# Kernel optimization log

Hardware: AMD Instinct MI355X
Metric: run time of the kernel (lower is better)

The kernel has to match this reference:

```python
import jax, jax.numpy as jnp
import numpy as np

B, T, D, U = 128, 512, 128, 512


def setup_inputs() -> dict:
    key = jax.random.key(0)
    kx, kwx, kwh = jax.random.split(key, 3)
    x = jax.random.normal(kx, (B, T, D), dtype=jnp.float32)
    Wx = jax.random.normal(kwx, (D, U), dtype=jnp.float32) * (1.0 / np.sqrt(D))
    Wh = jax.random.normal(kwh, (U, U), dtype=jnp.float32) * (1.0 / np.sqrt(U))
    b = jnp.zeros((U,), dtype=jnp.float32)
    return {"x": x, "Wx": Wx, "Wh": Wh, "b": b}


def reference(x, Wx, Wh, b):
    # Elman RNN: h_t = tanh(x_t @ Wx + h_{t-1} @ Wh + b)
    # Faithful to MyRNN(return_sequences=True): TensorArray.stack() -> [T, B, U]
    h0 = jnp.zeros((x.shape[0], Wh.shape[0]), dtype=x.dtype)  # fallback zero initial state
    xs = jnp.swapaxes(x, 0, 1)  # [T, B, D] for scan over time

    def step(h, x_t):
        h_new = jnp.tanh(x_t @ Wx + h @ Wh + b)
        return h_new, h_new

    _, seq = jax.lax.scan(step, h0, xs)
    return seq  # [T, B, U]
```

## Files before the change

kernel.cpp:

```cpp
#include <hip/hip_runtime.h>
#include <stddef.h>
#include <stdint.h>


constexpr int B = 128;
constexpr int T = 512;
constexpr int D = 128;
constexpr int U = 512;

typedef _Float16 f16;
typedef _Float16 f16x2 __attribute__((ext_vector_type(2)));
typedef __fp16   fp16x2 __attribute__((ext_vector_type(2)));
typedef unsigned int u32;
typedef u32 u32x16 __attribute__((ext_vector_type(16)));

union U32H2 { u32 u; f16x2 h; fp16x2 p; };

static __device__ __forceinline__ u32 pk(float a, float b) {
    U32H2 c; c.p = __builtin_amdgcn_cvt_pkrtz(a, b); return c.u;
}

#if __has_builtin(__builtin_amdgcn_fdot2)
static __device__ __forceinline__ float fdot2(u32 a, u32 b, float c) {
    U32H2 x, y; x.u = a; y.u = b;
    return __builtin_amdgcn_fdot2(x.h, y.h, c, false);
}
#else
static __device__ __forceinline__ float fdot2(u32 a, u32 b, float c) {
    U32H2 x, y; x.u = a; y.u = b;
    return c + (float)x.h.x * (float)y.h.x + (float)x.h.y * (float)y.h.y;
}
#endif

static __device__ __forceinline__ float fast_tanh(float x) {
    float e = __expf(2.0f * x);
    return 1.0f - 2.0f * __builtin_amdgcn_rcpf(e + 1.0f);
}

__global__ __launch_bounds__(256) void pgemm_kernel(
    const float* __restrict__ x,
    const float* __restrict__ Wx,
    const float* __restrict__ bias,
    float* __restrict__ P)
{
    __shared__ u32 xs[128][66];
    __shared__ u32 ws[64][132];

    const int rb  = blockIdx.x;
    const int cb  = blockIdx.y;
    const int tid = threadIdx.x;
    const int tr  = tid >> 4;
    const int tcc = tid & 15;

    const float4* x4 = (const float4*)x;
#pragma unroll
    for (int l = 0; l < 16; ++l) {
        int idx = tid + l * 256;
        int r   = idx >> 5;
        int q   = idx & 31;
        int m   = rb * 128 + r;
        int b_  = m & 127;
        int t_  = m >> 7;
        float4 v = x4[((size_t)b_ * T + t_) * 32 + q];
        xs[r][2 * q]     = pk(v.x, v.y);
        xs[r][2 * q + 1] = pk(v.z, v.w);
    }
    const float4* W4 = (const float4*)Wx;
#pragma unroll
    for (int l = 0; l < 8; ++l) {
        int idx = tid + l * 256;
        int kp  = idx >> 5;
        int q   = idx & 31;
        float4 a = W4[(size_t)(2 * kp)     * 128 + cb * 32 + q];
        float4 c = W4[(size_t)(2 * kp + 1) * 128 + cb * 32 + q];
        uint4 w;
        w.x = pk(a.x, c.x); w.y = pk(a.y, c.y);
        w.z = pk(a.z, c.z); w.w = pk(a.w, c.w);
        *(uint4*)&ws[kp][4 * q] = w;
    }
    __syncthreads();

    float acc[8][8];
#pragma unroll
    for (int i = 0; i < 8; ++i)
#pragma unroll
        for (int j = 0; j < 8; ++j) acc[i][j] = 0.f;

#pragma unroll 2
    for (int kp = 0; kp < 64; ++kp) {
        u32 xv[8], wv[8];
#pragma unroll
        for (int i = 0; i < 8; ++i) xv[i] = xs[tr + 16 * i][kp];
#pragma unroll
        for (int j = 0; j < 8; ++j) wv[j] = ws[kp][tcc + 16 * j];
#pragma unroll
        for (int i = 0; i < 8; ++i)
#pragma unroll
            for (int j = 0; j < 8; ++j)
                acc[i][j] = fdot2(xv[i], wv[j], acc[i][j]);
    }

#pragma unroll
    for (int j = 0; j < 8; ++j) {
        int c    = cb * 128 + tcc + 16 * j;
        float bv = bias[c];
#pragma unroll
        for (int i = 0; i < 8; ++i) {
            int m = rb * 128 + tr + 16 * i;
            P[(size_t)m * U + c] = acc[i][j] + bv;
        }
    }
}

__global__ __launch_bounds__(512, 2) void rnn_kernel(
    const float* __restrict__ Wh,
    float* __restrict__ out)
{
    __shared__ __align__(16) u32 WhL[32768];
    __shared__ __align__(16) u32 part[16 * 264];
    __shared__ __align__(16) u32 hbuf[320];

    const int tid = threadIdx.x;
    const int tk  = tid >> 5;
    const int tc  = tid & 31;
    const int b   = blockIdx.x;

    u32x16 W0, W1, W2, W3, W4, W5, W6, W7, W8, W9, W10, W11;
#define LOADW(q)                                                          \
    {                                                                     \
        const float* r0 = Wh + (size_t)((tk * 16 + (q)) * 2) * U + tc;    \
        _Pragma("unroll")                                                 \
        for (int j = 0; j < 16; ++j)                                      \
            W##q[j] = pk(r0[32 * j], r0[U + 32 * j]);                     \
    }
    LOADW(0)  LOADW(1)  LOADW(2)  LOADW(3)
    LOADW(4)  LOADW(5)  LOADW(6)  LOADW(7)
    LOADW(8)  LOADW(9)  LOADW(10) LOADW(11)
#undef LOADW

#pragma unroll
    for (int pl2 = 0; pl2 < 4; ++pl2) {
        const float* r0 = Wh + (size_t)((tk * 16 + 12 + pl2) * 2) * U + tc;
#pragma unroll
        for (int jc = 0; jc < 4; ++jc) {
            uint4 w;
            w.x = pk(r0[32 * (4 * jc + 0)], r0[U + 32 * (4 * jc + 0)]);
            w.y = pk(r0[32 * (4 * jc + 1)], r0[U + 32 * (4 * jc + 1)]);
            w.z = pk(r0[32 * (4 * jc + 2)], r0[U + 32 * (4 * jc + 2)]);
            w.w = pk(r0[32 * (4 * jc + 3)], r0[U + 32 * (4 * jc + 3)]);
            *(uint4*)&WhL[((pl2 * 4 + jc) * 512 + tid) * 4] = w;
        }
    }

    if (tid < 320) hbuf[tid] = 0u;
    __syncthreads();

    float* outb = out + (size_t)b * U;
    f16* hb16 = (f16*)hbuf;
    const int p0    = tid >> 1;
    const int hidx  = 2 * (p0 + 4 * (p0 >> 4)) + (tid & 1);

    float pv0 = 0.f, pv1 = 0.f;
    if (tid < 256) { pv0 = outb[tid]; pv1 = outb[tid + 256]; }

    for (int t = 0; t < T; ++t) {
        int tn = (t + 1 < T) ? (t + 1) : t;
        const float* prown = outb + (size_t)tn * (B * U);
        float nv0 = 0.f, nv1 = 0.f;
        if (tid < 256) { nv0 = prown[tid]; nv1 = prown[tid + 256]; }

        float acc[16];
#pragma unroll
        for (int j = 0; j < 16; ++j) acc[j] = 0.f;

        const uint4* h4p = (const uint4*)&hbuf[20 * tk];

#define DOT16(hq, Wq)                                                     \
        {                                                                 \
            u32 hq_ = (hq);                                               \
            _Pragma("unroll")                                             \
            for (int j = 0; j < 16; ++j)                                  \
                acc[j] = fdot2(hq_, Wq[j], acc[j]);                       \
        }
        { uint4 hv = h4p[0];
          DOT16(hv.x, W0) DOT16(hv.y, W1) DOT16(hv.z, W2) DOT16(hv.w, W3) }
        { uint4 hv = h4p[1];
          DOT16(hv.x, W4) DOT16(hv.y, W5) DOT16(hv.z, W6) DOT16(hv.w, W7) }
        { uint4 hv = h4p[2];
          DOT16(hv.x, W8) DOT16(hv.y, W9) DOT16(hv.z, W10) DOT16(hv.w, W11) }
#undef DOT16

        {
            uint4 hv = h4p[3];
#pragma unroll
            for (int pl2 = 0; pl2 < 4; ++pl2) {
                u32 hq = (pl2 == 0) ? hv.x : (pl2 == 1) ? hv.y
                       : (pl2 == 2) ? hv.z : hv.w;
#pragma unroll
                for (int jc = 0; jc < 4; ++jc) {
                    uint4 w = *(const uint4*)&WhL[((pl2 * 4 + jc) * 512 + tid) * 4];
                    acc[4 * jc + 0] = fdot2(hq, w.x, acc[4 * jc + 0]);
                    acc[4 * jc + 1] = fdot2(hq, w.y, acc[4 * jc + 1]);
                    acc[4 * jc + 2] = fdot2(hq, w.z, acc[4 * jc + 2]);
                    acc[4 * jc + 3] = fdot2(hq, w.w, acc[4 * jc + 3]);
                }
            }
        }

#pragma unroll
        for (int j = 0; j < 8; ++j)
            part[tk * 264 + tc + 32 * j] = pk(acc[j], acc[j + 8]);

        __syncthreads();

        if (tid < 256) {
            float s0 = pv0, s1 = pv1;
#pragma unroll
            for (int i = 0; i < 16; ++i) {
                U32H2 w; w.u = part[i * 264 + tid];
                s0 += (float)w.h.x;
                s1 += (float)w.h.y;
            }
            float h0 = fast_tanh(s0);
            float h1 = fast_tanh(s1);
            float* prow = outb + (size_t)t * (B * U);
            prow[tid]        = h0;
            prow[tid + 256]  = h1;
            hb16[hidx]       = (f16)h0;
            hb16[hidx + 320] = (f16)h1;
        }
        pv0 = nv0; pv1 = nv1;

        __syncthreads();
    }
}

extern "C" void kernel_launch(void* const* d_in, const int* in_sizes, int n_in,
                              void* d_out, int out_size, void* d_ws, size_t ws_size,
                              hipStream_t stream)
{
    (void)d_ws; (void)ws_size; (void)in_sizes; (void)n_in; (void)out_size;
    const float* x    = (const float*)d_in[0];
    const float* Wx   = (const float*)d_in[1];
    const float* Wh   = (const float*)d_in[2];
    const float* bias = (const float*)d_in[3];
    float* out = (float*)d_out;

    pgemm_kernel<<<dim3((T * B) / 128, U / 128), 256, 0, stream>>>(x, Wx, bias, out);
    rnn_kernel<<<B, 512, 0, stream>>>(Wh, out);
}
```

Before: 1.034 ms.

## Widen RNN recurrence to 1024 threads with 64-column groups and pipelined LDS weights

The recurrent kernel now runs 1024 threads per block instead of 512. Each thread holds half as many Wh register values (8 columns instead of 16) and the K dimension is split across 16 groups of 64 columns. LDS weight loads are issued ahead and interleaved with register dot products to hide LDS latency. The cross-group reduction becomes a tree sum, and h is packed with a lane shuffle so the padded hbuf indexing goes away. The aim is more waves to hide latency per serial time step, at the cost of more threads taking part in each barrier.

```diff
diff --git a/kernel.cpp b/kernel.cpp
--- a/kernel.cpp
+++ b/kernel.cpp
@@ -12,7 +12,7 @@
 typedef _Float16 f16x2 __attribute__((ext_vector_type(2)));
 typedef __fp16   fp16x2 __attribute__((ext_vector_type(2)));
 typedef unsigned int u32;
-typedef u32 u32x16 __attribute__((ext_vector_type(16)));
+typedef u32 u32x8 __attribute__((ext_vector_type(8)));
 
 union U32H2 { u32 u; f16x2 h; fp16x2 p; };
 
@@ -112,26 +112,28 @@
     }
 }
 
-__global__ __launch_bounds__(512, 2) void rnn_kernel(
+__global__ __launch_bounds__(1024)
+__attribute__((amdgpu_waves_per_eu(4, 4)))
+void rnn_kernel(
     const float* __restrict__ Wh,
     float* __restrict__ out)
 {
     __shared__ __align__(16) u32 WhL[32768];
-    __shared__ __align__(16) u32 part[16 * 264];
-    __shared__ __align__(16) u32 hbuf[320];
+    __shared__ __align__(16) u32 part[4096];
+    __shared__ __align__(16) u32 hbuf[256];
 
     const int tid = threadIdx.x;
-    const int tk  = tid >> 5;
-    const int tc  = tid & 31;
+    const int kg  = tid >> 6;
+    const int cg  = tid & 63;
     const int b   = blockIdx.x;
 
-    u32x16 W0, W1, W2, W3, W4, W5, W6, W7, W8, W9, W10, W11;
+    u32x8 W0, W1, W2, W3, W4, W5, W6, W7, W8, W9, W10, W11;
 #define LOADW(q)                                                          \
     {                                                                     \
-        const float* r0 = Wh + (size_t)((tk * 16 + (q)) * 2) * U + tc;    \
+        const float* r0 = Wh + (size_t)(32 * kg + 2 * (q)) * U + cg;      \
         _Pragma("unroll")                                                 \
-        for (int j = 0; j < 16; ++j)                                      \
-            W##q[j] = pk(r0[32 * j], r0[U + 32 * j]);                     \
+        for (int j = 0; j < 8; ++j)                                       \
+            W##q[j] = pk(r0[64 * j], r0[U + 64 * j]);                     \
     }
     LOADW(0)  LOADW(1)  LOADW(2)  LOADW(3)
     LOADW(4)  LOADW(5)  LOADW(6)  LOADW(7)
@@ -139,26 +141,24 @@
 #undef LOADW
 
 #pragma unroll
-    for (int pl2 = 0; pl2 < 4; ++pl2) {
-        const float* r0 = Wh + (size_t)((tk * 16 + 12 + pl2) * 2) * U + tc;
-#pragma unroll
-        for (int jc = 0; jc < 4; ++jc) {
+    for (int qq = 0; qq < 4; ++qq) {
+        const float* r0 = Wh + (size_t)(32 * kg + 24 + 2 * qq) * U + cg;
+#pragma unroll
+        for (int i = 0; i < 2; ++i) {
             uint4 w;
-            w.x = pk(r0[32 * (4 * jc + 0)], r0[U + 32 * (4 * jc + 0)]);
-            w.y = pk(r0[32 * (4 * jc + 1)], r0[U + 32 * (4 * jc + 1)]);
-            w.z = pk(r0[32 * (4 * jc + 2)], r0[U + 32 * (4 * jc + 2)]);
-            w.w = pk(r0[32 * (4 * jc + 3)], r0[U + 32 * (4 * jc + 3)]);
-            *(uint4*)&WhL[((pl2 * 4 + jc) * 512 + tid) * 4] = w;
-        }
-    }
-
-    if (tid < 320) hbuf[tid] = 0u;
+            w.x = pk(r0[64 * (4 * i + 0)], r0[U + 64 * (4 * i + 0)]);
+            w.y = pk(r0[64 * (4 * i + 1)], r0[U + 64 * (4 * i + 1)]);
+            w.z = pk(r0[64 * (4 * i + 2)], r0[U + 64 * (4 * i + 2)]);
+            w.w = pk(r0[64 * (4 * i + 3)], r0[U + 64 * (4 * i + 3)]);
+            *(uint4*)&WhL[(size_t)(qq * 2 + i) * 4096 + tid * 4] = w;
+        }
+    }
+
+    if (tid < 256) hbuf[tid] = 0u;
     __syncthreads();
 
+    const uint4* WL4 = (const uint4*)WhL;
     float* outb = out + (size_t)b * U;
-    f16* hb16 = (f16*)hbuf;
-    const int p0    = tid >> 1;
-    const int hidx  = 2 * (p0 + 4 * (p0 >> 4)) + (tid & 1);
 
     float pv0 = 0.f, pv1 = 0.f;
     if (tid < 256) { pv0 = outb[tid]; pv1 = outb[tid + 256]; }
@@ -169,69 +169,95 @@
         float nv0 = 0.f, nv1 = 0.f;
         if (tid < 256) { nv0 = prown[tid]; nv1 = prown[tid + 256]; }
 
-        float acc[16];
-#pragma unroll
-        for (int j = 0; j < 16; ++j) acc[j] = 0.f;
-
-        const uint4* h4p = (const uint4*)&hbuf[20 * tk];
-
-#define DOT16(hq, Wq)                                                     \
+        const uint4* hb4 = (const uint4*)hbuf;
+        uint4 h0 = hb4[4 * kg + 0];
+        uint4 h1 = hb4[4 * kg + 1];
+        uint4 h2 = hb4[4 * kg + 2];
+        uint4 h3 = hb4[4 * kg + 3];
+
+        uint4 wlA = WL4[0 * 1024 + tid], wlB = WL4[1 * 1024 + tid];
+        uint4 wlC = WL4[2 * 1024 + tid], wlD = WL4[3 * 1024 + tid];
+
+        float acc[8];
+#pragma unroll
+        for (int j = 0; j < 8; ++j) acc[j] = 0.f;
+
+#define DOT8(hq, Wq)                                                      \
         {                                                                 \
             u32 hq_ = (hq);                                               \
             _Pragma("unroll")                                             \
-            for (int j = 0; j < 16; ++j)                                  \
+            for (int j = 0; j < 8; ++j)                                   \
                 acc[j] = fdot2(hq_, Wq[j], acc[j]);                       \
         }
-        { uint4 hv = h4p[0];
-          DOT16(hv.x, W0) DOT16(hv.y, W1) DOT16(hv.z, W2) DOT16(hv.w, W3) }
-        { uint4 hv = h4p[1];
-          DOT16(hv.x, W4) DOT16(hv.y, W5) DOT16(hv.z, W6) DOT16(hv.w, W7) }
-        { uint4 hv = h4p[2];
-          DOT16(hv.x, W8) DOT16(hv.y, W9) DOT16(hv.z, W10) DOT16(hv.w, W11) }
-#undef DOT16
-
-        {
-            uint4 hv = h4p[3];
-#pragma unroll
-            for (int pl2 = 0; pl2 < 4; ++pl2) {
-                u32 hq = (pl2 == 0) ? hv.x : (pl2 == 1) ? hv.y
-                       : (pl2 == 2) ? hv.z : hv.w;
-#pragma unroll
-                for (int jc = 0; jc < 4; ++jc) {
-                    uint4 w = *(const uint4*)&WhL[((pl2 * 4 + jc) * 512 + tid) * 4];
-                    acc[4 * jc + 0] = fdot2(hq, w.x, acc[4 * jc + 0]);
-                    acc[4 * jc + 1] = fdot2(hq, w.y, acc[4 * jc + 1]);
-                    acc[4 * jc + 2] = fdot2(hq, w.z, acc[4 * jc + 2]);
-                    acc[4 * jc + 3] = fdot2(hq, w.w, acc[4 * jc + 3]);
+#define CONSUME8(hq, Aq, Bq)                                              \
+        {                                                                 \
+            u32 hq_ = (hq);                                               \
+            acc[0] = fdot2(hq_, Aq.x, acc[0]);                            \
+            acc[1] = fdot2(hq_, Aq.y, acc[1]);                            \
+            acc[2] = fdot2(hq_, Aq.z, acc[2]);                            \
+            acc[3] = fdot2(hq_, Aq.w, acc[3]);                            \
+            acc[4] = fdot2(hq_, Bq.x, acc[4]);                            \
+            acc[5] = fdot2(hq_, Bq.y, acc[5]);                            \
+            acc[6] = fdot2(hq_, Bq.z, acc[6]);                            \
+            acc[7] = fdot2(hq_, Bq.w, acc[7]);                            \
+        }
+        DOT8(h0.x, W0) DOT8(h0.y, W1) DOT8(h0.z, W2) DOT8(h0.w, W3)
+        DOT8(h1.x, W4) DOT8(h1.y, W5)
+
+        CONSUME8(h3.x, wlA, wlB)
+        wlA = WL4[4 * 1024 + tid]; wlB = WL4[5 * 1024 + tid];
+
+        DOT8(h1.z, W6) DOT8(h1.w, W7) DOT8(h2.x, W8) DOT8(h2.y, W9)
+
+        CONSUME8(h3.y, wlC, wlD)
+        wlC = WL4[6 * 1024 + tid]; wlD = WL4[7 * 1024 + tid];
+
+        DOT8(h2.z, W10) DOT8(h2.w, W11)
+
+        CONSUME8(h3.z, wlA, wlB)
+        CONSUME8(h3.w, wlC, wlD)
+#undef CONSUME8
+#undef DOT8
+
+#pragma unroll
+        for (int j = 0; j < 4; ++j)
+            part[kg * 256 + cg + 64 * j] = pk(acc[j], acc[j + 4]);
+
+        __syncthreads();
+
+        if (tid < 256) {
+            float a0[16], a1[16];
+#pragma unroll
+            for (int i = 0; i < 16; ++i) {
+                U32H2 w; w.u = part[i * 256 + tid];
+                a0[i] = (float)w.h.x;
+                a1[i] = (float)w.h.y;
+            }
+            float s0 = pv0, s1 = pv1;
+#pragma unroll
+            for (int d = 1; d < 16; d <<= 1)
+#pragma unroll
+                for (int i = 0; i < 16; i += 2 * d) {
+                    a0[i] += a0[i + d];
+                    a1[i] += a1[i + d];
                 }
+            s0 += a0[0];
+            s1 += a1[0];
+            float h0v = fast_tanh(s0);
+            float h1v = fast_tanh(s1);
+            float* prow = outb + (size_t)t * (B * U);
+            prow[tid]       = h0v;
+            prow[tid + 256] = h1v;
+            float o0 = __shfl_xor(h0v, 1);
+            float o1 = __shfl_xor(h1v, 1);
+            if (!(tid & 1)) {
+                hbuf[tid >> 1]         = pk(h0v, o0);
+                hbuf[128 + (tid >> 1)] = pk(h1v, o1);
             }
         }
 
-#pragma unroll
-        for (int j = 0; j < 8; ++j)
-            part[tk * 264 + tc + 32 * j] = pk(acc[j], acc[j + 8]);
-
         __syncthreads();
-
-        if (tid < 256) {
-            float s0 = pv0, s1 = pv1;
-#pragma unroll
-            for (int i = 0; i < 16; ++i) {
-                U32H2 w; w.u = part[i * 264 + tid];
-                s0 += (float)w.h.x;
-                s1 += (float)w.h.y;
-            }
-            float h0 = fast_tanh(s0);
-            float h1 = fast_tanh(s1);
-            float* prow = outb + (size_t)t * (B * U);
-            prow[tid]        = h0;
-            prow[tid + 256]  = h1;
-            hb16[hidx]       = (f16)h0;
-            hb16[hidx + 320] = (f16)h1;
-        }
         pv0 = nv0; pv1 = nv1;
-
-        __syncthreads();
     }
 }
 
@@ -247,5 +273,5 @@
     float* out = (float*)d_out;
 
     pgemm_kernel<<<dim3((T * B) / 128, U / 128), 256, 0, stream>>>(x, Wx, bias, out);
-    rnn_kernel<<<B, 512, 0, stream>>>(Wh, out);
-}
+    rnn_kernel<<<B, 1024, 0, stream>>>(Wh, out);
+}
```

New measurement: 1.445 ms. 39.8% more time.

## Use MFMA for recurrent matvec with per-wave column ownership and double-buffered h

Applied to the files above, without the earlier changes.

Replaces the fdot2-based recurrent step with MFMA 16x16x32 f16 instructions. Each wave owns 64 output columns over the full K range, so the shared-memory partial-sum reduction stage and one barrier per step go away. Only row 0 of the A operand holds h and the other rows are zeroed, which wastes most of the MFMA throughput in exchange for not reducing across waves. The hidden state is double-buffered in shared memory so a single sync per timestep is enough. The next timestep's precomputed input is now loaded after the tanh, which may expose global-load latency.

```diff
diff --git a/kernel.cpp b/kernel.cpp
--- a/kernel.cpp
+++ b/kernel.cpp
@@ -10,9 +10,10 @@
 
 typedef _Float16 f16;
 typedef _Float16 f16x2 __attribute__((ext_vector_type(2)));
+typedef _Float16 f16x8 __attribute__((ext_vector_type(8)));
 typedef __fp16   fp16x2 __attribute__((ext_vector_type(2)));
+typedef float    f32x4 __attribute__((ext_vector_type(4)));
 typedef unsigned int u32;
-typedef u32 u32x16 __attribute__((ext_vector_type(16)));
 
 union U32H2 { u32 u; f16x2 h; fp16x2 p; };
 
@@ -116,122 +117,119 @@
     const float* __restrict__ Wh,
     float* __restrict__ out)
 {
-    __shared__ __align__(16) u32 WhL[32768];
-    __shared__ __align__(16) u32 part[16 * 264];
-    __shared__ __align__(16) u32 hbuf[320];
+    __shared__ __align__(16) u32 WL[32768];
+    __shared__ __align__(16) u32 hbuf[2][256];
 
     const int tid = threadIdx.x;
-    const int tk  = tid >> 5;
-    const int tc  = tid & 31;
+    const int w   = tid >> 6;
+    const int l   = tid & 63;
+    const int lg  = l >> 4;
+    const int lc  = l & 15;
     const int b   = blockIdx.x;
 
-    u32x16 W0, W1, W2, W3, W4, W5, W6, W7, W8, W9, W10, W11;
-#define LOADW(q)                                                          \
-    {                                                                     \
-        const float* r0 = Wh + (size_t)((tk * 16 + (q)) * 2) * U + tc;    \
-        _Pragma("unroll")                                                 \
-        for (int j = 0; j < 16; ++j)                                      \
-            W##q[j] = pk(r0[32 * j], r0[U + 32 * j]);                     \
-    }
-    LOADW(0)  LOADW(1)  LOADW(2)  LOADW(3)
-    LOADW(4)  LOADW(5)  LOADW(6)  LOADW(7)
-    LOADW(8)  LOADW(9)  LOADW(10) LOADW(11)
-#undef LOADW
-
-#pragma unroll
-    for (int pl2 = 0; pl2 < 4; ++pl2) {
-        const float* r0 = Wh + (size_t)((tk * 16 + 12 + pl2) * 2) * U + tc;
-#pragma unroll
-        for (int jc = 0; jc < 4; ++jc) {
-            uint4 w;
-            w.x = pk(r0[32 * (4 * jc + 0)], r0[U + 32 * (4 * jc + 0)]);
-            w.y = pk(r0[32 * (4 * jc + 1)], r0[U + 32 * (4 * jc + 1)]);
-            w.z = pk(r0[32 * (4 * jc + 2)], r0[U + 32 * (4 * jc + 2)]);
-            w.w = pk(r0[32 * (4 * jc + 3)], r0[U + 32 * (4 * jc + 3)]);
-            *(uint4*)&WhL[((pl2 * 4 + jc) * 512 + tid) * 4] = w;
-        }
-    }
-
-    if (tid < 320) hbuf[tid] = 0u;
+    f16x8 Wf[4][12];
+#pragma unroll
+    for (int ct = 0; ct < 4; ++ct) {
+#pragma unroll
+        for (int s = 0; s < 12; ++s) {
+            const float* src = Wh + (size_t)(32 * s + 8 * lg) * U
+                             + 64 * w + 16 * ct + lc;
+            f16x8 f;
+#pragma unroll
+            for (int e = 0; e < 8; ++e) f[e] = (f16)src[(size_t)e * U];
+            Wf[ct][s] = f;
+        }
+    }
+#pragma unroll
+    for (int sr = 0; sr < 4; ++sr) {
+#pragma unroll
+        for (int ct = 0; ct < 4; ++ct) {
+            const float* src = Wh + (size_t)(32 * (12 + sr) + 8 * lg) * U
+                             + 64 * w + 16 * ct + lc;
+            f16x8 f;
+#pragma unroll
+            for (int e = 0; e < 8; ++e) f[e] = (f16)src[(size_t)e * U];
+            *(f16x8*)&WL[((w * 16 + sr * 4 + ct) * 64 + l) * 4] = f;
+        }
+    }
+
+    if (tid < 256) { hbuf[0][tid] = 0u; hbuf[1][tid] = 0u; }
     __syncthreads();
 
     float* outb = out + (size_t)b * U;
-    f16* hb16 = (f16*)hbuf;
-    const int p0    = tid >> 1;
-    const int hidx  = 2 * (p0 + 4 * (p0 >> 4)) + (tid & 1);
-
-    float pv0 = 0.f, pv1 = 0.f;
-    if (tid < 256) { pv0 = outb[tid]; pv1 = outb[tid + 256]; }
+
+    float pv0 = 0.f, pv1 = 0.f, pv2 = 0.f, pv3 = 0.f;
+    if (l < 16) {
+        pv0 = outb[64 * w + 0  + lc];
+        pv1 = outb[64 * w + 16 + lc];
+        pv2 = outb[64 * w + 32 + lc];
+        pv3 = outb[64 * w + 48 + lc];
+    }
 
     for (int t = 0; t < T; ++t) {
-        int tn = (t + 1 < T) ? (t + 1) : t;
-        const float* prown = outb + (size_t)tn * (B * U);
-        float nv0 = 0.f, nv1 = 0.f;
-        if (tid < 256) { nv0 = prown[tid]; nv1 = prown[tid + 256]; }
-
-        float acc[16];
-#pragma unroll
-        for (int j = 0; j < 16; ++j) acc[j] = 0.f;
-
-        const uint4* h4p = (const uint4*)&hbuf[20 * tk];
-
-#define DOT16(hq, Wq)                                                     \
-        {                                                                 \
-            u32 hq_ = (hq);                                               \
-            _Pragma("unroll")                                             \
-            for (int j = 0; j < 16; ++j)                                  \
-                acc[j] = fdot2(hq_, Wq[j], acc[j]);                       \
-        }
-        { uint4 hv = h4p[0];
-          DOT16(hv.x, W0) DOT16(hv.y, W1) DOT16(hv.z, W2) DOT16(hv.w, W3) }
-        { uint4 hv = h4p[1];
-          DOT16(hv.x, W4) DOT16(hv.y, W5) DOT16(hv.z, W6) DOT16(hv.w, W7) }
-        { uint4 hv = h4p[2];
-          DOT16(hv.x, W8) DOT16(hv.y, W9) DOT16(hv.z, W10) DOT16(hv.w, W11) }
-#undef DOT16
-
-        {
-            uint4 hv = h4p[3];
-#pragma unroll
-            for (int pl2 = 0; pl2 < 4; ++pl2) {
-                u32 hq = (pl2 == 0) ? hv.x : (pl2 == 1) ? hv.y
-                       : (pl2 == 2) ? hv.z : hv.w;
-#pragma unroll
-                for (int jc = 0; jc < 4; ++jc) {
-                    uint4 w = *(const uint4*)&WhL[((pl2 * 4 + jc) * 512 + tid) * 4];
-                    acc[4 * jc + 0] = fdot2(hq, w.x, acc[4 * jc + 0]);
-                    acc[4 * jc + 1] = fdot2(hq, w.y, acc[4 * jc + 1]);
-                    acc[4 * jc + 2] = fdot2(hq, w.z, acc[4 * jc + 2]);
-                    acc[4 * jc + 3] = fdot2(hq, w.w, acc[4 * jc + 3]);
-                }
-            }
-        }
-
-#pragma unroll
-        for (int j = 0; j < 8; ++j)
-            part[tk * 264 + tc + 32 * j] = pk(acc[j], acc[j + 8]);
+        const int par = t & 1;
+        const f16* hb = (const f16*)hbuf[par];
+
+        f32x4 acc0 = (f32x4)0.f, acc1 = (f32x4)0.f;
+        f32x4 acc2 = (f32x4)0.f, acc3 = (f32x4)0.f;
+
+#define ALOAD(s)                                                          \
+        ({                                                                \
+            f16x8 a_ = (f16x8)0;                                          \
+            if (lc == 0)                                                  \
+                a_ = *(const f16x8*)&hb[32 * (s) + 8 * lg];               \
+            a_;                                                           \
+        })
+
+#pragma unroll
+        for (int s = 0; s < 12; ++s) {
+            f16x8 a = ALOAD(s);
+            acc0 = __builtin_amdgcn_mfma_f32_16x16x32_f16(a, Wf[0][s], acc0, 0, 0, 0);
+            acc1 = __builtin_amdgcn_mfma_f32_16x16x32_f16(a, Wf[1][s], acc1, 0, 0, 0);
+            acc2 = __builtin_amdgcn_mfma_f32_16x16x32_f16(a, Wf[2][s], acc2, 0, 0, 0);
+            acc3 = __builtin_amdgcn_mfma_f32_16x16x32_f16(a, Wf[3][s], acc3, 0, 0, 0);
+        }
+#pragma unroll
+        for (int sr = 0; sr < 4; ++sr) {
+            f16x8 a = ALOAD(12 + sr);
+            f16x8 b0 = *(const f16x8*)&WL[((w * 16 + sr * 4 + 0) * 64 + l) * 4];
+            f16x8 b1 = *(const f16x8*)&WL[((w * 16 + sr * 4 + 1) * 64 + l) * 4];
+            f16x8 b2 = *(const f16x8*)&WL[((w * 16 + sr * 4 + 2) * 64 + l) * 4];
+            f16x8 b3 = *(const f16x8*)&WL[((w * 16 + sr * 4 + 3) * 64 + l) * 4];
+            acc0 = __builtin_amdgcn_mfma_f32_16x16x32_f16(a, b0, acc0, 0, 0, 0);
+            acc1 = __builtin_amdgcn_mfma_f32_16x16x32_f16(a, b1, acc1, 0, 0, 0);
+            acc2 = __builtin_amdgcn_mfma_f32_16x16x32_f16(a, b2, acc2, 0, 0, 0);
+            acc3 = __builtin_amdgcn_mfma_f32_16x16x32_f16(a, b3, acc3, 0, 0, 0);
+        }
+#undef ALOAD
+
+        float nv0 = 0.f, nv1 = 0.f, nv2 = 0.f, nv3 = 0.f;
+        if (l < 16) {
+            float* prow = outb + (size_t)t * (B * U);
+            const float* prown = outb + (size_t)((t + 1 < T) ? t + 1 : t) * (B * U);
+            f16* hbn = (f16*)hbuf[par ^ 1];
+
+            float h0 = fast_tanh(pv0 + acc0.x);
+            float h1 = fast_tanh(pv1 + acc1.x);
+            float h2 = fast_tanh(pv2 + acc2.x);
+            float h3 = fast_tanh(pv3 + acc3.x);
+            prow[64 * w + 0  + lc] = h0;
+            prow[64 * w + 16 + lc] = h1;
+            prow[64 * w + 32 + lc] = h2;
+            prow[64 * w + 48 + lc] = h3;
+            hbn[64 * w + 0  + lc] = (f16)h0;
+            hbn[64 * w + 16 + lc] = (f16)h1;
+            hbn[64 * w + 32 + lc] = (f16)h2;
+            hbn[64 * w + 48 + lc] = (f16)h3;
+
+            nv0 = prown[64 * w + 0  + lc];
+            nv1 = prown[64 * w + 16 + lc];
+            nv2 = prown[64 * w + 32 + lc];
+            nv3 = prown[64 * w + 48 + lc];
+        }
 
         __syncthreads();
-
-        if (tid < 256) {
-            float s0 = pv0, s1 = pv1;
-#pragma unroll
-            for (int i = 0; i < 16; ++i) {
-                U32H2 w; w.u = part[i * 264 + tid];
-                s0 += (float)w.h.x;
-                s1 += (float)w.h.y;
-            }
-            float h0 = fast_tanh(s0);
-            float h1 = fast_tanh(s1);
-            float* prow = outb + (size_t)t * (B * U);
-            prow[tid]        = h0;
-            prow[tid + 256]  = h1;
-            hb16[hidx]       = (f16)h0;
-            hb16[hidx + 320] = (f16)h1;
-        }
-        pv0 = nv0; pv1 = nv1;
-
-        __syncthreads();
+        pv0 = nv0; pv1 = nv1; pv2 = nv2; pv3 = nv3;
     }
 }
 
```

Measured after the change: 997.6 us. 1.04x faster.
